# Kernel optimization log

Measured on AMD Instinct MI355X. Metric: run time of the kernel, lower is better.

The kernel has to match this reference:

```python
import jax, jax.numpy as jnp
import numpy as np

EPS = 1e-8
B, L, D = 8, 2048, 128

def _l2norm(x):
    # F.normalize-style: x / max(||x||, eps)
    n = jnp.sqrt(jnp.sum(x * x, axis=-1, keepdims=True))
    return x / jnp.maximum(n, EPS)

def setup_inputs() -> dict:
    key = jax.random.key(0)
    k0, k1, k2, k3, k4 = jax.random.split(key, 5)
    context = jax.random.normal(k0, (B, 2, L, D), dtype=jnp.float32)
    # MlpModule (BLINK-style): Linear(D, D) -> ReLU -> Linear(D, 1)
    W1 = jax.random.normal(k1, (D, D), dtype=jnp.float32) * (1.0 / np.sqrt(D))
    b1 = jnp.zeros((D,), dtype=jnp.float32)
    W2 = jax.random.normal(k2, (D, 1), dtype=jnp.float32) * (1.0 / np.sqrt(D))
    b2 = jnp.zeros((1,), dtype=jnp.float32)
    return {"context": context, "W1": W1, "b1": b1, "W2": W2, "b2": b2}

def reference(context, W1, b1, W2, b2):
    ctx = context[:, 0]          # [B, L, D] mention-side tokens
    ent = context[:, 1]          # [B, L, D] entity-side tokens
    cn = _l2norm(ctx)
    en = _l2norm(ent)
    # cosine similarity matrix [B, L, L]
    sim = jnp.einsum("bld,bmd->blm", cn, en)
    idx = jnp.argmax(sim, axis=-1)                          # [B, L]
    matched = jnp.take_along_axis(en, idx[..., None], axis=1)  # [B, L, D]
    pair = jnp.stack([cn, matched], axis=-2)                # [B, L, 2, D]
    h = jax.nn.relu(pair @ W1 + b1)                         # [B, L, 2, D]
    out = h @ W2 + b2                                       # [B, L, 2, 1]
    return jnp.sum(out, axis=-2).squeeze(-1)                # [B, L]
```

## Files before the change

### kernel.cpp

```cpp
#include <hip/hip_runtime.h>
#include <hip/hip_bf16.h>

#define B_ 8
#define L_ 2048
#define D_ 128
#define BL_ (B_ * L_)
#define DELTA2 0.016f
#define QCAP 4096

typedef __attribute__((ext_vector_type(8))) short bf16x8;
typedef __attribute__((ext_vector_type(4))) float f32x4;

__device__ __forceinline__ void gload_lds16(const void* g, void* l) {
    __builtin_amdgcn_global_load_lds(
        (const __attribute__((address_space(1))) unsigned int*)g,
        (__attribute__((address_space(3))) unsigned int*)l, 16, 0, 0);
}

#define WAIT_VM(N) asm volatile("s_waitcnt vmcnt(" #N ")" ::: "memory")

__global__ void k_norm(const float* __restrict__ ctx,
                       float* __restrict__ cn, float* __restrict__ en,
                       ushort* __restrict__ cnb, ushort* __restrict__ enb) {
    int bid  = blockIdx.x;
    int b    = bid & 7;
    int j    = bid >> 3;
    int idx  = j * 4 + (threadIdx.x >> 6);
    int lane = threadIdx.x & 63;
    int c    = idx >> 11;
    int l    = idx & 2047;

    const float* src = ctx + (((size_t)b * 2 + c) * L_ + l) * D_;
    float2 v = ((const float2*)src)[lane];
    float ss = v.x * v.x + v.y * v.y;
    #pragma unroll
    for (int off = 32; off; off >>= 1) ss += __shfl_down(ss, off, 64);
    ss = __shfl(ss, 0, 64);
    float n = fmaxf(sqrtf(ss), 1e-8f);
    float ox = v.x / n, oy = v.y / n;

    size_t ro = (size_t)(b * L_ + l) * D_;
    float* dst = (c == 0 ? cn : en) + ro;
    ((float2*)dst)[lane] = make_float2(ox, oy);

    __hip_bfloat16 hx = __float2bfloat16(ox), hy = __float2bfloat16(oy);
    ushort ux = *(ushort*)&hx, uy = *(ushort*)&hy;
    ushort* dstb = (c == 0 ? cnb : enb) + ro;
    ((ushort2*)dstb)[lane] = make_ushort2(ux, uy);
}

__global__ __launch_bounds__(512, 2) void k_sim(const ushort* __restrict__ cnb,
                                                const ushort* __restrict__ enb,
                                                const float* __restrict__ cn,
                                                const float* __restrict__ en,
                                                int* __restrict__ finalidx) {
    __shared__ __align__(16) char Bsm[8][4][4096];
    __shared__ float wrowmax[8][64];
    __shared__ float rowth_l[64];
    __shared__ unsigned long long best[64];
    __shared__ int qbuf[QCAP];
    __shared__ int qn;

    const int bid = blockIdx.x;
    const int b = bid & 7, rb = bid >> 3;
    const int row0 = rb * 64;
    const int tid = threadIdx.x;
    const int wave = tid >> 6, lane = tid & 63;
    const int m = lane & 15, q = lane >> 4;

    if (tid == 0) qn = 0;
    if (tid < 64) best[tid] = 0ULL;

    const ushort* Ab = cnb + ((size_t)(b * L_) + row0) * D_;
    const char* gw = (const char*)(enb + (size_t)(b * L_) * D_) + (size_t)wave * 65536;
    char* Bw = &Bsm[wave][0][0];

    bf16x8 Areg[16];
    #pragma unroll
    for (int rt = 0; rt < 4; ++rt)
        #pragma unroll
        for (int kc = 0; kc < 4; ++kc)
            Areg[rt * 4 + kc] = *(const bf16x8*)(Ab + (size_t)(rt * 16 + m) * D_ + kc * 32 + q * 8);

    auto STAGE = [&](int c) {
        const char* gc = gw + (size_t)c * 4096;
        char* lbuf = Bw + (c & 3) * 4096;
        #pragma unroll
        for (int i = 0; i < 4; ++i) {
            int j = i * 4 + q;
            int so = j * 256 + ((m ^ (j & 7)) << 4);
            gload_lds16(gc + so, lbuf + i * 1024);
        }
    };
    auto TILE = [&](int c, f32x4 acc[4]) {
        const char* lbuf = Bw + (c & 3) * 4096;
        #pragma unroll
        for (int rt = 0; rt < 4; ++rt) acc[rt] = (f32x4){0.f, 0.f, 0.f, 0.f};
        #pragma unroll
        for (int kc = 0; kc < 4; ++kc) {
            bf16x8 bf = *(const bf16x8*)(lbuf + m * 256 + ((kc * 64 + q * 16) ^ ((m & 7) << 4)));
            #pragma unroll
            for (int rt = 0; rt < 4; ++rt)
                acc[rt] = __builtin_amdgcn_mfma_f32_16x16x32_bf16(Areg[rt * 4 + kc], bf, acc[rt], 0, 0, 0);
        }
    };

    float runmax[16];
    #pragma unroll
    for (int s = 0; s < 16; ++s) runmax[s] = -3.0e38f;

    auto FMAX = [&](const f32x4 acc[4]) {
        #pragma unroll
        for (int rt = 0; rt < 4; ++rt)
            #pragma unroll
            for (int reg = 0; reg < 4; ++reg)
                runmax[rt * 4 + reg] = fmaxf(runmax[rt * 4 + reg], acc[rt][reg]);
    };

    STAGE(0); STAGE(1); STAGE(2);
    #pragma unroll 1
    for (int c = 0; c < 14; ++c) {
        WAIT_VM(8);
        f32x4 acc[4];
        TILE(c, acc);
        if (c < 13) STAGE(c + 3);
        FMAX(acc);
    }
    { WAIT_VM(4); f32x4 acc[4]; TILE(14, acc); FMAX(acc); }
    { WAIT_VM(0); f32x4 acc[4]; TILE(15, acc); FMAX(acc); }

    #pragma unroll
    for (int s = 0; s < 16; ++s) {
        float v = runmax[s];
        v = fmaxf(v, __shfl_xor(v, 1, 64));
        v = fmaxf(v, __shfl_xor(v, 2, 64));
        v = fmaxf(v, __shfl_xor(v, 4, 64));
        v = fmaxf(v, __shfl_xor(v, 8, 64));
        runmax[s] = v;
    }
    if (m == 0) {
        #pragma unroll
        for (int rt = 0; rt < 4; ++rt)
            #pragma unroll
            for (int reg = 0; reg < 4; ++reg)
                wrowmax[wave][rt * 16 + q * 4 + reg] = runmax[rt * 4 + reg];
    }
    __syncthreads();
    if (tid < 64) {
        float rm = wrowmax[0][tid];
        #pragma unroll
        for (int w = 1; w < 8; ++w) rm = fmaxf(rm, wrowmax[w][tid]);
        rowth_l[tid] = rm - DELTA2;
    }
    __syncthreads();
    float rowth_r[16];
    #pragma unroll
    for (int rt = 0; rt < 4; ++rt)
        #pragma unroll
        for (int reg = 0; reg < 4; ++reg)
            rowth_r[rt * 4 + reg] = rowth_l[rt * 16 + q * 4 + reg];

    auto CAPT = [&](int c, const f32x4 acc[4]) {
        int col = wave * 256 + c * 16 + m;
        #pragma unroll
        for (int rt = 0; rt < 4; ++rt)
            #pragma unroll
            for (int reg = 0; reg < 4; ++reg)
                if (acc[rt][reg] >= rowth_r[rt * 4 + reg]) {
                    int row = rt * 16 + q * 4 + reg;
                    int pos = atomicAdd(&qn, 1);
                    if (pos < QCAP) qbuf[pos] = (row << 12) | col;
                }
    };

    #pragma unroll 1
    for (int d = 0; d < 4; ++d) {
        f32x4 acc[4];
        TILE(15 - d, acc);
        STAGE(11 - d);
        CAPT(15 - d, acc);
    }
    #pragma unroll 1
    for (int d = 4; d < 13; ++d) {
        WAIT_VM(12);
        f32x4 acc[4];
        TILE(15 - d, acc);
        if (d < 12) STAGE(11 - d);
        CAPT(15 - d, acc);
    }
    { WAIT_VM(8); f32x4 acc[4]; TILE(2, acc); CAPT(2, acc); }
    { WAIT_VM(4); f32x4 acc[4]; TILE(1, acc); CAPT(1, acc); }
    { WAIT_VM(0); f32x4 acc[4]; TILE(0, acc); CAPT(0, acc); }
    __syncthreads();

    int qtot = min(qn, QCAP);
    for (int e0 = wave * 4; e0 < qtot; e0 += 32) {
        int e = e0 + q;
        bool act = (e < qtot);
        int pc = qbuf[act ? e : (qtot - 1)];
        int rl = (pc >> 12) & 63, col = pc & 0xFFF;
        const float* ar = cn + ((size_t)(b * L_) + row0 + rl) * D_;
        const float* br = en + ((size_t)(b * L_) + col) * D_;
        float4 x0 = ((const float4*)ar)[m * 2], x1 = ((const float4*)ar)[m * 2 + 1];
        float4 y0 = ((const float4*)br)[m * 2], y1 = ((const float4*)br)[m * 2 + 1];
        double s = (double)x0.x * y0.x + (double)x0.y * y0.y +
                   (double)x0.z * y0.z + (double)x0.w * y0.w +
                   (double)x1.x * y1.x + (double)x1.y * y1.y +
                   (double)x1.z * y1.z + (double)x1.w * y1.w;
        s += __shfl_xor(s, 1, 64);
        s += __shfl_xor(s, 2, 64);
        s += __shfl_xor(s, 4, 64);
        s += __shfl_xor(s, 8, 64);
        if (act && m == 0) {
            unsigned long long ub = (unsigned long long)__double_as_longlong(s);
            ub = (ub & 0x8000000000000000ULL) ? ~ub : (ub | 0x8000000000000000ULL);
            ub = (ub & ~0x7FFULL) | (unsigned long long)(2047 - col);
            atomicMax(&best[rl], ub);
        }
    }
    __syncthreads();
    if (tid < 64)
        finalidx[b * L_ + row0 + tid] = 2047 - (int)(best[tid] & 0x7FFULL);
}

__global__ __launch_bounds__(256) void k_mlp(
        const float* __restrict__ cn, const float* __restrict__ en,
        const int* __restrict__ finalidx,
        const float* __restrict__ W1, const float* __restrict__ b1,
        const float* __restrict__ W2, const float* __restrict__ b2,
        float* __restrict__ out) {
    __shared__ __align__(16) float As[32][132];
    __shared__ __align__(16) float Bs[32][132];
    __shared__ float redv[128][16];
    __shared__ float sumv[128];
    __shared__ int fidxs[64];

    int tid = threadIdx.x;
    int tx = tid & 15, ty = tid >> 4;
    int r  = tid >> 3, kg = tid & 7;
    int bid = blockIdx.x;
    int b = bid & 7, rb = bid >> 3;
    int row0 = rb * 64;

    if (tid < 64) fidxs[tid] = finalidx[b * L_ + row0 + tid];

    const float* cnb_ = cn + ((size_t)(b * L_) + row0) * D_;
    const float* enb_ = en + (size_t)(b * L_) * D_;

    float acc[8][8];
    #pragma unroll
    for (int i = 0; i < 8; ++i)
        #pragma unroll
        for (int j = 0; j < 8; ++j) acc[i][j] = 0.0f;

    for (int kc = 0; kc < 4; ++kc) {
        __syncthreads();
        #pragma unroll
        for (int p = 0; p < 4; ++p) {
            int rr = r + 32 * p;
            const float* srow = (rr < 64) ? (cnb_ + (size_t)rr * D_)
                                          : (enb_ + (size_t)fidxs[rr - 64] * D_);
            float4 v = *(const float4*)(srow + kc * 32 + kg * 4);
            As[kg][rr]      = v.x;
            As[8 + kg][rr]  = v.y;
            As[16 + kg][rr] = v.z;
            As[24 + kg][rr] = v.w;
        }
        {
            int kr = r, phys = (kr & 3) * 8 + (kr >> 2);
            const float* srcp = W1 + (size_t)(kc * 32 + kr) * D_ + kg * 16;
            #pragma unroll
            for (int qq = 0; qq < 4; ++qq)
                *(float4*)&Bs[phys][kg * 16 + qq * 4] = *(const float4*)(srcp + qq * 4);
        }
        __syncthreads();
        #pragma unroll
        for (int k = 0; k < 32; ++k) {
            float a[8], bb[8];
            *(float4*)&a[0]  = *(const float4*)&As[k][ty * 4];
            *(float4*)&a[4]  = *(const float4*)&As[k][64 + ty * 4];
            *(float4*)&bb[0] = *(const float4*)&Bs[k][tx * 4];
            *(float4*)&bb[4] = *(const float4*)&Bs[k][64 + tx * 4];
            #pragma unroll
            for (int i = 0; i < 8; ++i)
                #pragma unroll
                for (int j = 0; j < 8; ++j)
                    acc[i][j] = fmaf(a[i], bb[j], acc[i][j]);
        }
    }

    float w2j[8], b1j[8];
    #pragma unroll
    for (int jj = 0; jj < 8; ++jj) {
        int c = (jj < 4) ? (tx * 4 + jj) : (64 + tx * 4 + (jj - 4));
        w2j[jj] = W2[c];
        b1j[jj] = b1[c];
    }
    float bias2 = b2[0];
    __syncthreads();
    #pragma unroll
    for (int i = 0; i < 8; ++i) {
        float s = 0.0f;
        #pragma unroll
        for (int jj = 0; jj < 8; ++jj)
            s += fmaxf(acc[i][jj] + b1j[jj], 0.0f) * w2j[jj];
        int rowl = (i < 4) ? (ty * 4 + i) : (64 + ty * 4 + (i - 4));
        redv[rowl][tx] = s;
    }
    __syncthreads();
    if (tid < 128) {
        float s = 0.0f;
        #pragma unroll
        for (int tt = 0; tt < 16; ++tt) s += redv[tid][tt];
        sumv[tid] = s + bias2;
    }
    __syncthreads();
    if (tid < 64)
        out[b * L_ + row0 + tid] = sumv[tid] + sumv[64 + tid];
}

extern "C" void kernel_launch(void* const* d_in, const int* in_sizes, int n_in,
                              void* d_out, int out_size, void* d_ws, size_t ws_size,
                              hipStream_t stream) {
    const float* context = (const float*)d_in[0];
    const float* W1 = (const float*)d_in[1];
    const float* b1 = (const float*)d_in[2];
    const float* W2 = (const float*)d_in[3];
    const float* b2 = (const float*)d_in[4];
    float* out = (float*)d_out;

    char* ws = (char*)d_ws;
    float*  cn  = (float*)(ws);
    float*  en  = (float*)(ws + 8388608);
    ushort* cnb = (ushort*)(ws + 16777216);
    ushort* enb = (ushort*)(ws + 20971520);
    int* finalidx = (int*)(ws + 25296896);

    k_norm<<<8192, 256, 0, stream>>>(context, cn, en, cnb, enb);
    k_sim<<<256, 512, 0, stream>>>(cnb, enb, cn, en, finalidx);
    k_mlp<<<256, 256, 0, stream>>>(cn, en, finalidx, W1, b1, W2, b2, out);
}
```

Before: 129.3 us.

## Split sim column sweep across 16 waves with double-buffered LDS ring

```diff
diff --git a/kernel.cpp b/kernel.cpp
--- a/kernel.cpp
+++ b/kernel.cpp
@@ -6,7 +6,7 @@
 #define D_ 128
 #define BL_ (B_ * L_)
 #define DELTA2 0.016f
-#define QCAP 4096
+#define QCAP 1024
 
 typedef __attribute__((ext_vector_type(8))) short bf16x8;
 typedef __attribute__((ext_vector_type(4))) float f32x4;
@@ -22,15 +22,14 @@
 __global__ void k_norm(const float* __restrict__ ctx,
                        float* __restrict__ cn, float* __restrict__ en,
                        ushort* __restrict__ cnb, ushort* __restrict__ enb) {
-    int bid  = blockIdx.x;
-    int b    = bid & 7;
-    int j    = bid >> 3;
-    int idx  = j * 4 + (threadIdx.x >> 6);
+    int wid  = blockIdx.x * 4 + (threadIdx.x >> 6);
     int lane = threadIdx.x & 63;
-    int c    = idx >> 11;
-    int l    = idx & 2047;
-
-    const float* src = ctx + (((size_t)b * 2 + c) * L_ + l) * D_;
+    int b   = wid >> 12;
+    int rem = wid & 4095;
+    int c   = rem >> 11;
+    int l   = rem & 2047;
+
+    const float* src = ctx + (size_t)wid * D_;
     float2 v = ((const float2*)src)[lane];
     float ss = v.x * v.x + v.y * v.y;
     #pragma unroll
@@ -49,13 +48,12 @@
     ((ushort2*)dstb)[lane] = make_ushort2(ux, uy);
 }
 
-__global__ __launch_bounds__(512, 2) void k_sim(const ushort* __restrict__ cnb,
-                                                const ushort* __restrict__ enb,
-                                                const float* __restrict__ cn,
-                                                const float* __restrict__ en,
-                                                int* __restrict__ finalidx) {
-    __shared__ __align__(16) char Bsm[8][4][4096];
-    __shared__ float wrowmax[8][64];
+__global__ __launch_bounds__(1024, 4) void k_sim(
+        const ushort* __restrict__ cnb, const ushort* __restrict__ enb,
+        const float* __restrict__ cn,  const float* __restrict__ en,
+        int* __restrict__ finalidx) {
+    __shared__ __align__(16) char ring[16][2][4096];
+    __shared__ float wrowmax[16][64];
     __shared__ float rowth_l[64];
     __shared__ unsigned long long best[64];
     __shared__ int qbuf[QCAP];
@@ -72,8 +70,8 @@
     if (tid < 64) best[tid] = 0ULL;
 
     const ushort* Ab = cnb + ((size_t)(b * L_) + row0) * D_;
-    const char* gw = (const char*)(enb + (size_t)(b * L_) * D_) + (size_t)wave * 65536;
-    char* Bw = &Bsm[wave][0][0];
+    const char* gw = (const char*)(enb + (size_t)(b * L_) * D_) + (size_t)wave * 32768;
+    char* Bw = &ring[wave][0][0];
 
     bf16x8 Areg[16];
     #pragma unroll
@@ -84,7 +82,7 @@
 
     auto STAGE = [&](int c) {
         const char* gc = gw + (size_t)c * 4096;
-        char* lbuf = Bw + (c & 3) * 4096;
+        char* lbuf = Bw + (c & 1) * 4096;
         #pragma unroll
         for (int i = 0; i < 4; ++i) {
             int j = i * 4 + q;
@@ -93,7 +91,7 @@
         }
     };
     auto TILE = [&](int c, f32x4 acc[4]) {
-        const char* lbuf = Bw + (c & 3) * 4096;
+        const char* lbuf = Bw + (c & 1) * 4096;
         #pragma unroll
         for (int rt = 0; rt < 4; ++rt) acc[rt] = (f32x4){0.f, 0.f, 0.f, 0.f};
         #pragma unroll
@@ -117,17 +115,17 @@
                 runmax[rt * 4 + reg] = fmaxf(runmax[rt * 4 + reg], acc[rt][reg]);
     };
 
-    STAGE(0); STAGE(1); STAGE(2);
+    STAGE(0); STAGE(1);
     #pragma unroll 1
-    for (int c = 0; c < 14; ++c) {
-        WAIT_VM(8);
+    for (int c = 0; c < 6; ++c) {
+        WAIT_VM(4);
         f32x4 acc[4];
         TILE(c, acc);
-        if (c < 13) STAGE(c + 3);
+        STAGE(c + 2);
         FMAX(acc);
     }
-    { WAIT_VM(4); f32x4 acc[4]; TILE(14, acc); FMAX(acc); }
-    { WAIT_VM(0); f32x4 acc[4]; TILE(15, acc); FMAX(acc); }
+    { WAIT_VM(4); f32x4 acc[4]; TILE(6, acc); FMAX(acc); }
+    { WAIT_VM(0); f32x4 acc[4]; TILE(7, acc); FMAX(acc); }
 
     #pragma unroll
     for (int s = 0; s < 16; ++s) {
@@ -149,7 +147,7 @@
     if (tid < 64) {
         float rm = wrowmax[0][tid];
         #pragma unroll
-        for (int w = 1; w < 8; ++w) rm = fmaxf(rm, wrowmax[w][tid]);
+        for (int w = 1; w < 16; ++w) rm = fmaxf(rm, wrowmax[w][tid]);
         rowth_l[tid] = rm - DELTA2;
     }
     __syncthreads();
@@ -161,7 +159,7 @@
             rowth_r[rt * 4 + reg] = rowth_l[rt * 16 + q * 4 + reg];
 
     auto CAPT = [&](int c, const f32x4 acc[4]) {
-        int col = wave * 256 + c * 16 + m;
+        int col = wave * 128 + c * 16 + m;
         #pragma unroll
         for (int rt = 0; rt < 4; ++rt)
             #pragma unroll
@@ -173,28 +171,22 @@
                 }
     };
 
+    { f32x4 acc[4]; TILE(7, acc); STAGE(5); CAPT(7, acc); }
+    { f32x4 acc[4]; TILE(6, acc); STAGE(4); CAPT(6, acc); }
     #pragma unroll 1
-    for (int d = 0; d < 4; ++d) {
+    for (int d = 2; d < 6; ++d) {
+        WAIT_VM(4);
         f32x4 acc[4];
-        TILE(15 - d, acc);
-        STAGE(11 - d);
-        CAPT(15 - d, acc);
-    }
-    #pragma unroll 1
-    for (int d = 4; d < 13; ++d) {
-        WAIT_VM(12);
-        f32x4 acc[4];
-        TILE(15 - d, acc);
-        if (d < 12) STAGE(11 - d);
-        CAPT(15 - d, acc);
-    }
-    { WAIT_VM(8); f32x4 acc[4]; TILE(2, acc); CAPT(2, acc); }
+        TILE(7 - d, acc);
+        STAGE(5 - d);
+        CAPT(7 - d, acc);
+    }
     { WAIT_VM(4); f32x4 acc[4]; TILE(1, acc); CAPT(1, acc); }
     { WAIT_VM(0); f32x4 acc[4]; TILE(0, acc); CAPT(0, acc); }
     __syncthreads();
 
     int qtot = min(qn, QCAP);
-    for (int e0 = wave * 4; e0 < qtot; e0 += 32) {
+    for (int e0 = wave * 4; e0 < qtot; e0 += 64) {
         int e = e0 + q;
         bool act = (e < qtot);
         int pc = qbuf[act ? e : (qtot - 1)];
@@ -334,9 +326,9 @@
     float*  en  = (float*)(ws + 8388608);
     ushort* cnb = (ushort*)(ws + 16777216);
     ushort* enb = (ushort*)(ws + 20971520);
-    int* finalidx = (int*)(ws + 25296896);
+    int* finalidx = (int*)(ws + 25165824);
 
     k_norm<<<8192, 256, 0, stream>>>(context, cn, en, cnb, enb);
-    k_sim<<<256, 512, 0, stream>>>(cnb, enb, cn, en, finalidx);
+    k_sim<<<256, 1024, 0, stream>>>(cnb, enb, cn, en, finalidx);
     k_mlp<<<256, 256, 0, stream>>>(cn, en, finalidx, W1, b1, W2, b2, out);
 }
```

Measured after the change: 135.2 us. 4.6% more time.
